# Optimization experiments

Hardware: AMD Instinct MI355X
Metric: run time of the kernel (lower is better)

The kernel has to match this reference:

```python
import jax, jax.numpy as jnp
import numpy as np

NUM_HEAD = 16
D_MODEL = 1024


def setup_inputs() -> dict:
    key = jax.random.key(0)
    ks = jax.random.split(key, 11)
    B, S, D = 2, 2048, D_MODEL
    scale = 1.0 / np.sqrt(D)
    inp = {
        "q": jax.random.normal(ks[0], (B, S, D), dtype=jnp.float32),
        "k": jax.random.normal(ks[1], (B, S, D), dtype=jnp.float32),
        "v": jax.random.normal(ks[2], (B, S, D), dtype=jnp.float32),
        "Wq": jax.random.normal(ks[3], (D, D), dtype=jnp.float32) * scale,
        "bq": jnp.zeros((D,), dtype=jnp.float32),
        "Wk": jax.random.normal(ks[4], (D, D), dtype=jnp.float32) * scale,
        "bk": jnp.zeros((D,), dtype=jnp.float32),
        "Wv": jax.random.normal(ks[5], (D, D), dtype=jnp.float32) * scale,
        "bv": jnp.zeros((D,), dtype=jnp.float32),
        "Wo": jax.random.normal(ks[6], (D, D), dtype=jnp.float32) * scale,
        "bo": jnp.zeros((D,), dtype=jnp.float32),
    }
    return inp


def _split_heads(x, num_head):
    B, S, D = x.shape
    return x.reshape(B, S, num_head, D // num_head).transpose(0, 2, 1, 3)  # [B,H,S,d]


def reference(q, k, v, Wq, bq, Wk, bk, Wv, bv, Wo, bo):
    H = NUM_HEAD
    qp = q @ Wq + bq
    kp = k @ Wk + bk  # computed but UNUSED, matching source bug
    vp = v @ Wv + bv
    # source bug: k := split_heads(v-projection)
    qh = _split_heads(qp, H)          # [B,H,S,d]
    kh = _split_heads(vp, H)          # [B,H,S,d]  (v-projection used as keys)
    vh = _split_heads(vp, H)          # [B,H,S,d]
    d = qh.shape[-1]
    scores = jnp.einsum('bhqd,bhkd->bhqk', qh, kh) / jnp.sqrt(jnp.asarray(d, qh.dtype))
    attn = jax.nn.softmax(scores, axis=-1)
    out = jnp.einsum('bhqk,bhkd->bhqd', attn, vh)  # [B,H,S,d]
    B, _, S, _ = out.shape
    out = out.transpose(0, 2, 1, 3).reshape(B, S, H * d)
    return out @ Wo + bo
```

## Files before the change

### kernel.cpp

```cpp
#include <hip/hip_runtime.h>
#include <hip/hip_bf16.h>

using bfrag  = __attribute__((ext_vector_type(8))) __bf16;
using f32x4  = __attribute__((ext_vector_type(4))) float;
using f32x16 = __attribute__((ext_vector_type(16))) float;
using v4u    = __attribute__((ext_vector_type(4))) unsigned int;
using v2u    = __attribute__((ext_vector_type(2))) unsigned int;

__device__ __forceinline__ ushort f2bf(float f) {
    union { float f; unsigned u; } c; c.f = f;
    return (ushort)((c.u + 0x7fffu + ((c.u >> 16) & 1u)) >> 16);
}

__device__ __forceinline__ float bf2f(ushort u) {
    union { unsigned u; float f; } c; c.u = (unsigned)u << 16; return c.f;
}

__device__ __forceinline__ unsigned pack_bf16x2(float lo, float hi) {
    union { __hip_bfloat162 h; unsigned u; } c;
    c.h = __float22bfloat162_rn(make_float2(lo, hi));
    return c.u;
}

__device__ __forceinline__ void gld_lds16(const ushort* g, ushort* l) {
    __builtin_amdgcn_global_load_lds(
        (const __attribute__((address_space(1))) void*)g,
        (__attribute__((address_space(3))) void*)l, 16, 0, 0);
}

__device__ __forceinline__ f32x16 mfma32(bfrag a, bfrag b, f32x16 c) {
    return __builtin_amdgcn_mfma_f32_32x32x16_bf16(a, b, c, 0, 0, 0);
}


__global__ void cvt_all(const float* __restrict__ s0, ushort* __restrict__ d0,
                        const float* __restrict__ s1, ushort* __restrict__ d1,
                        const float* __restrict__ s2, ushort* __restrict__ d2,
                        const float* __restrict__ q, ushort* __restrict__ qbf,
                        const float* __restrict__ v, ushort* __restrict__ vbf) {
    const int z = blockIdx.z;
    if (z < 3) {
        __shared__ float t[32][33];
        const float* src = z == 0 ? s0 : z == 1 ? s1 : s2;
        ushort* dst = z == 0 ? d0 : z == 1 ? d1 : d2;
        const int tx = threadIdx.x, ty = threadIdx.y;
        const int c0 = blockIdx.x * 32, r0 = blockIdx.y * 32;
        for (int i = ty; i < 32; i += 8) t[i][tx] = src[(size_t)(r0 + i) * 1024 + c0 + tx];
        __syncthreads();
        for (int i = ty; i < 32; i += 8) dst[(size_t)(c0 + i) * 1024 + r0 + tx] = f2bf(t[tx][i]);
    } else {
        const int tid = threadIdx.y * 32 + threadIdx.x;
        int i = ((z - 3) * 1024 + blockIdx.y * 32 + blockIdx.x) * 256 + tid;
        const float* s; ushort* d;
        if (i < 1048576) { s = q; d = qbf; } else { s = v; d = vbf; i -= 1048576; }
        float4 f = ((const float4*)s)[i];
        ((ushort4*)d)[i] = make_ushort4(f2bf(f.x), f2bf(f.y), f2bf(f.z), f2bf(f.w));
    }
}


__global__ __launch_bounds__(256, 3) void gemm_qv(
    const ushort* __restrict__ Aq, const ushort* __restrict__ Wq, const float* __restrict__ bq, ushort* __restrict__ Cq,
    const ushort* __restrict__ Av, const ushort* __restrict__ Wv, const float* __restrict__ bv, ushort* __restrict__ Cv,
    ushort* __restrict__ VPT, float qscale)
{
    __shared__ ushort SM[12288];
    const int z = blockIdx.z;
    const ushort* A  = z ? Av : Aq;
    const ushort* Bt = z ? Wv : Wq;
    const float* bias = z ? bv : bq;
    ushort* Cout = z ? Cv : Cq;
    const float scale = z ? 1.0f : qscale;

    const int tid = threadIdx.x;
    const int lane = tid & 63, w = tid >> 6;
    const int l15 = lane & 15, lg = lane >> 4;
    const int wr = w >> 1, wc = w & 1;
    const int bM = blockIdx.y, bN = blockIdx.x;

    const ushort* Ag = A + (size_t)bM * 64 * 1024;
    const ushort* Bg = Bt + (size_t)bN * 128 * 1024;
    const int ar = tid >> 2;
    const int cc = (tid & 3) * 8;

    auto STAGE = [&](int buf, int kt) {
        const int kk = kt * 32;
        gld_lds16(Ag + (size_t)ar * 1024 + kk + cc, &SM[buf * 2048 + tid * 8]);
#pragma unroll
        for (int i = 0; i < 2; ++i)
            gld_lds16(Bg + (size_t)(ar + i * 64) * 1024 + kk + cc,
                      &SM[4096 + buf * 4096 + (tid + i * 256) * 8]);
    };

    f32x4 acc[2][4];
#pragma unroll
    for (int m = 0; m < 2; ++m)
#pragma unroll
        for (int n = 0; n < 4; ++n) acc[m][n] = (f32x4){0.f, 0.f, 0.f, 0.f};

    STAGE(0, 0);
    __syncthreads();
    int cur = 0;
    for (int kt = 0; kt < 32; ++kt) {
        if (kt < 31) STAGE(cur ^ 1, kt + 1);
        bfrag aF[2], bF[4];
#pragma unroll
        for (int m = 0; m < 2; ++m)
            aF[m] = *(const bfrag*)&SM[cur * 2048 + (wr * 32 + m * 16 + l15) * 32 + lg * 8];
#pragma unroll
        for (int n = 0; n < 4; ++n)
            bF[n] = *(const bfrag*)&SM[4096 + cur * 4096 + (wc * 64 + n * 16 + l15) * 32 + lg * 8];
        __builtin_amdgcn_s_setprio(1);
#pragma unroll
        for (int m = 0; m < 2; ++m)
#pragma unroll
            for (int n = 0; n < 4; ++n)
                acc[m][n] = __builtin_amdgcn_mfma_f32_16x16x32_bf16(aF[m], bF[n], acc[m][n], 0, 0, 0);
        __builtin_amdgcn_s_setprio(0);
        if (kt < 31) {
            __syncthreads();
            cur ^= 1;
        }
    }

    __syncthreads();
#pragma unroll
    for (int m = 0; m < 2; ++m)
#pragma unroll
        for (int n = 0; n < 4; ++n) {
            const int lcol = wc * 64 + n * 16 + l15;
            const int gcol = bN * 128 + lcol;
            const float bv_ = bias[gcol];
#pragma unroll
            for (int j = 0; j < 4; ++j) {
                const int lrow = wr * 32 + m * 16 + lg * 4 + j;
                const float val = (acc[m][n][j] + bv_) * scale;
                const ushort hv = f2bf(val);
                Cout[(size_t)(bM * 64 + lrow) * 1024 + gcol] = hv;
                if (z) SM[lrow * 129 + lcol] = hv;
            }
        }

    if (z) {
        __syncthreads();
        const int b_ = (bM * 64) >> 11;
        const int s0 = (bM * 64) & 2047;
        const int h0 = bN * 2;
#pragma unroll
        for (int i = 0; i < 4; ++i) {
            const int c2 = i * 256 + tid;
            const int d128 = c2 >> 3;
            const int sb = (c2 & 7) * 8;
            union { ushort s[8]; v4u v; } tmp;
#pragma unroll
            for (int jj = 0; jj < 8; ++jj) {
                const int sl = sb + jj;
                const int js = (sl & ~15) | (sl & 3) | ((sl >> 1) & 4) | ((sl << 1) & 8);
                tmp.s[jj] = SM[js * 129 + d128];
            }
            ushort* dst = VPT + ((size_t)((b_ * 16 + h0 + (d128 >> 6)) * 64 + (d128 & 63))) * 2048 + s0 + sb;
            *(v4u*)dst = tmp.v;
        }
    }
}


__global__ __launch_bounds__(256, 3) void gemm_o(
    const ushort* __restrict__ Op0, const ushort* __restrict__ Op1,
    const float* __restrict__ Lp,
    const ushort* __restrict__ Bt, const float* __restrict__ bias,
    float* __restrict__ out)
{
    __shared__ ushort As[2][2048];
    __shared__ ushort Bs[2][4096];
    const int tid = threadIdx.x;
    const int lane = tid & 63, w = tid >> 6;
    const int l15 = lane & 15, lg = lane >> 4;
    const int wr = w >> 1, wc = w & 1;
    const int bM = blockIdx.y, bN = blockIdx.x;

    const ushort* Bg = Bt + (size_t)bN * 128 * 1024;
    const int ar = tid >> 2;
    const int cc = (tid & 3) * 8;
    const int grow = bM * 64 + ar;
    const int b_ = grow >> 11, s_ = grow & 2047;

    v4u aR, cR; float inv;
    auto LOAD_A = [&](int kt) {
        const int col = kt * 32 + cc;
        const int li = (b_ * 16 + (col >> 6)) * 2048 + s_;
        inv = 1.0f / (Lp[li] + Lp[65536 + li]);
        aR = *(const v4u*)(Op0 + (size_t)grow * 1024 + col);
        cR = *(const v4u*)(Op1 + (size_t)grow * 1024 + col);
    };
    auto WRITE_A = [&](int buf) {
        v4u o;
#pragma unroll
        for (int wd = 0; wd < 4; ++wd) {
            const float x0 = (bf2f((ushort)(aR[wd] & 0xffff)) + bf2f((ushort)(cR[wd] & 0xffff))) * inv;
            const float x1 = (bf2f((ushort)(aR[wd] >> 16))    + bf2f((ushort)(cR[wd] >> 16)))    * inv;
            o[wd] = pack_bf16x2(x0, x1);
        }
        *(v4u*)&As[buf][tid * 8] = o;
    };
    auto STAGE_B = [&](int buf, int kt) {
        const int kk = kt * 32;
#pragma unroll
        for (int i = 0; i < 2; ++i)
            gld_lds16(Bg + (size_t)(ar + i * 64) * 1024 + kk + cc, &Bs[buf][(tid + i * 256) * 8]);
    };

    f32x4 acc[2][4];
#pragma unroll
    for (int m = 0; m < 2; ++m)
#pragma unroll
        for (int n = 0; n < 4; ++n) acc[m][n] = (f32x4){0.f, 0.f, 0.f, 0.f};

    LOAD_A(0);
    STAGE_B(0, 0);
    WRITE_A(0);
    __syncthreads();
    int cur = 0;
    for (int kt = 0; kt < 32; ++kt) {
        if (kt < 31) {
            LOAD_A(kt + 1);
            STAGE_B(cur ^ 1, kt + 1);
        }
        bfrag aF[2], bF[4];
#pragma unroll
        for (int m = 0; m < 2; ++m) aF[m] = *(const bfrag*)&As[cur][(wr * 32 + m * 16 + l15) * 32 + lg * 8];
#pragma unroll
        for (int n = 0; n < 4; ++n) bF[n] = *(const bfrag*)&Bs[cur][(wc * 64 + n * 16 + l15) * 32 + lg * 8];
        __builtin_amdgcn_s_setprio(1);
#pragma unroll
        for (int m = 0; m < 2; ++m)
#pragma unroll
            for (int n = 0; n < 4; ++n)
                acc[m][n] = __builtin_amdgcn_mfma_f32_16x16x32_bf16(aF[m], bF[n], acc[m][n], 0, 0, 0);
        __builtin_amdgcn_s_setprio(0);
        if (kt < 31) {
            WRITE_A(cur ^ 1);
            __syncthreads();
            cur ^= 1;
        }
    }

#pragma unroll
    for (int m = 0; m < 2; ++m)
#pragma unroll
        for (int n = 0; n < 4; ++n) {
            const int gcol = bN * 128 + wc * 64 + n * 16 + l15;
            const float bv_ = bias[gcol];
#pragma unroll
            for (int j = 0; j < 4; ++j) {
                const int gr = bM * 64 + wr * 32 + m * 16 + lg * 4 + j;
                out[(size_t)gr * 1024 + gcol] = acc[m][n][j] + bv_;
            }
        }
}


__global__ __launch_bounds__(256, 2) void attn_kernel(
    const ushort* __restrict__ QP, const ushort* __restrict__ VP,
    const ushort* __restrict__ VPT, ushort* __restrict__ Opart, float* __restrict__ Lpart)
{
    __shared__ ushort Ks[2][4096];
    __shared__ ushort Vs[2][4096];
    const int tid = threadIdx.x;
    const int w = tid >> 6, lane = tid & 63;
    const int l31 = lane & 31, hi = lane >> 5;
    const int bh = blockIdx.x, qt = blockIdx.y, half = blockIdx.z;
    const int b = bh >> 4, h = bh & 15;
    const int qrow0 = qt * 256 + w * 64;
    const int k0 = half * 16;

    const int sr = lane >> 3;
    const int sc = ((lane & 7) ^ sr) * 8;
    const ushort* Kg = VP + (size_t)(b * 2048) * 1024 + h * 64 + sc;
    const ushort* Vg = VPT + (size_t)bh * 131072 + sc;

    auto STAGE = [&](int slot, int kt) {
#pragma unroll
        for (int i = 0; i < 2; ++i) {
            const int kb = w * 2 + i;
            const int r = kb * 8 + sr;
            gld_lds16(Kg + (size_t)(kt * 64 + r) * 1024, &Ks[slot][kb * 512]);
            gld_lds16(Vg + (size_t)r * 2048 + kt * 64, &Vs[slot][kb * 512]);
        }
    };

    const ushort* Qp = QP + ((size_t)(b * 2048 + qrow0 + l31)) * 1024 + h * 64 + hi * 8;
    bfrag qA[4], qBt[4];
#pragma unroll
    for (int ds = 0; ds < 4; ++ds) {
        qA[ds]  = *(const bfrag*)(Qp + ds * 16);
        qBt[ds] = *(const bfrag*)(Qp + 32 * 1024 + ds * 16);
    }

    f32x16 OA0, OA1, OB0, OB1;
#pragma unroll
    for (int r = 0; r < 16; ++r) { OA0[r] = 0.f; OA1[r] = 0.f; OB0[r] = 0.f; OB1[r] = 0.f; }
    float lrunA = 0.f, lrunB = 0.f;

    const int swz = (l31 & 7) << 4;
    const int cA = hi * 16;

    STAGE(0, k0);
    __syncthreads();

    auto SOFTMAX = [&](f32x16& S0, f32x16& S1, bfrag (&pB)[4], float& lrun) {
        float p[32];
#pragma unroll
        for (int r = 0; r < 16; ++r) {
            p[r]      = __builtin_amdgcn_exp2f(S0[r]);
            p[16 + r] = __builtin_amdgcn_exp2f(S1[r]);
        }
        float s8[8];
#pragma unroll
        for (int i = 0; i < 8; ++i) s8[i] = (p[i] + p[i + 8]) + (p[i + 16] + p[i + 24]);
        lrun += ((s8[0] + s8[1]) + (s8[2] + s8[3])) + ((s8[4] + s8[5]) + (s8[6] + s8[7]));
#pragma unroll
        for (int c = 0; c < 4; ++c) {
            union { v4u u; bfrag f; } cv;
#pragma unroll
            for (int wd = 0; wd < 4; ++wd)
                cv.u[wd] = pack_bf16x2(p[8 * c + 2 * wd], p[8 * c + 2 * wd + 1]);
            pB[c] = cv.f;
        }
    };

#pragma unroll 1
    for (int t = 0; t < 16; ++t) {
        if (t > 0) __syncthreads();
        if (t + 1 < 16) STAGE((t + 1) & 1, k0 + t + 1);
        const ushort* Kb_ = Ks[t & 1];
        const ushort* Vb_ = Vs[t & 1];

        bfrag k0f[4], k1f[4];
#pragma unroll
        for (int ds = 0; ds < 4; ++ds) {
            k0f[ds] = *(const bfrag*)&Kb_[(l31 * 128 + ((ds * 32 + cA) ^ swz)) >> 1];
            k1f[ds] = *(const bfrag*)&Kb_[((l31 + 32) * 128 + ((ds * 32 + cA) ^ swz)) >> 1];
        }
        f32x16 SA0, SA1, SB0, SB1;
#pragma unroll
        for (int r = 0; r < 16; ++r) { SA0[r] = -16.f; SA1[r] = -16.f; SB0[r] = -16.f; SB1[r] = -16.f; }
        __builtin_amdgcn_s_setprio(1);
#pragma unroll
        for (int ds = 0; ds < 4; ++ds) {
            SA0 = mfma32(k0f[ds], qA[ds], SA0);
            SA1 = mfma32(k1f[ds], qA[ds], SA1);
            SB0 = mfma32(k0f[ds], qBt[ds], SB0);
            SB1 = mfma32(k1f[ds], qBt[ds], SB1);
        }
        __builtin_amdgcn_s_setprio(0);

        bfrag pBA[4], pBB[4];
        SOFTMAX(SA0, SA1, pBA, lrunA);
        SOFTMAX(SB0, SB1, pBB, lrunB);

        bfrag vF0[4], vF1[4];
#pragma unroll
        for (int c = 0; c < 4; ++c) {
            vF0[c] = *(const bfrag*)&Vb_[(l31 * 128 + ((c * 32 + cA) ^ swz)) >> 1];
            vF1[c] = *(const bfrag*)&Vb_[((l31 + 32) * 128 + ((c * 32 + cA) ^ swz)) >> 1];
        }
        __builtin_amdgcn_s_setprio(1);
#pragma unroll
        for (int c = 0; c < 4; ++c) {
            OA0 = mfma32(vF0[c], pBA[c], OA0);
            OA1 = mfma32(vF1[c], pBA[c], OA1);
            OB0 = mfma32(vF0[c], pBB[c], OB0);
            OB1 = mfma32(vF1[c], pBB[c], OB1);
        }
        __builtin_amdgcn_s_setprio(0);
    }

    lrunA += __shfl_xor(lrunA, 32);
    lrunB += __shfl_xor(lrunB, 32);
    ushort* AoA = Opart + (size_t)half * 4194304
                + (size_t)(b * 2048 + qrow0 + l31) * 1024 + h * 64 + hi * 4;
    ushort* AoB = AoA + 32 * 1024;
#pragma unroll
    for (int t = 0; t < 2; ++t) {
#pragma unroll
        for (int g = 0; g < 4; ++g) {
            const float a0 = t ? OA1[4 * g + 0] : OA0[4 * g + 0];
            const float a1 = t ? OA1[4 * g + 1] : OA0[4 * g + 1];
            const float a2 = t ? OA1[4 * g + 2] : OA0[4 * g + 2];
            const float a3 = t ? OA1[4 * g + 3] : OA0[4 * g + 3];
            *(v2u*)(AoA + t * 32 + g * 8) = (v2u){pack_bf16x2(a0, a1), pack_bf16x2(a2, a3)};
            const float b0 = t ? OB1[4 * g + 0] : OB0[4 * g + 0];
            const float b1 = t ? OB1[4 * g + 1] : OB0[4 * g + 1];
            const float b2 = t ? OB1[4 * g + 2] : OB0[4 * g + 2];
            const float b3 = t ? OB1[4 * g + 3] : OB0[4 * g + 3];
            *(v2u*)(AoB + t * 32 + g * 8) = (v2u){pack_bf16x2(b0, b1), pack_bf16x2(b2, b3)};
        }
    }
    if (hi == 0) {
        Lpart[half * 65536 + bh * 2048 + qrow0 + l31] = lrunA;
        Lpart[half * 65536 + bh * 2048 + qrow0 + 32 + l31] = lrunB;
    }
}


extern "C" void kernel_launch(void* const* d_in, const int* in_sizes, int n_in,
                              void* d_out, int out_size, void* d_ws, size_t ws_size,
                              hipStream_t stream) {
    (void)in_sizes; (void)n_in; (void)out_size; (void)ws_size;
    const float* q  = (const float*)d_in[0];
    const float* v  = (const float*)d_in[2];
    const float* Wq = (const float*)d_in[3];
    const float* bq = (const float*)d_in[4];
    const float* Wv = (const float*)d_in[7];
    const float* bv = (const float*)d_in[8];
    const float* Wo = (const float*)d_in[9];
    const float* bo = (const float*)d_in[10];
    float* out = (float*)d_out;
    char* ws = (char*)d_ws;
    const size_t MB = 1ull << 20;
    ushort* qbf = (ushort*)(ws + 0);
    ushort* vbf = (ushort*)(ws + 8 * MB);
    ushort* WqT = (ushort*)(ws + 16 * MB);
    ushort* WvT = (ushort*)(ws + 18 * MB);
    ushort* WoT = (ushort*)(ws + 20 * MB);
    ushort* QPb = (ushort*)(ws + 22 * MB);
    ushort* VPb = (ushort*)(ws + 30 * MB);
    ushort* VPT = (ushort*)(ws + 38 * MB);

    ushort* Opart = (ushort*)(ws + 0);
    float*  Lpart = (float*)(ws + 16 * MB);

    cvt_all<<<dim3(32, 32, 11), dim3(32, 8), 0, stream>>>(
        Wq, WqT, Wv, WvT, Wo, WoT, q, qbf, v, vbf);

    const float qscale = 0.125f * 1.44269504088896340736f;
    gemm_qv<<<dim3(8, 64, 2), 256, 0, stream>>>(qbf, WqT, bq, QPb,
                                                vbf, WvT, bv, VPb, VPT, qscale);
    attn_kernel<<<dim3(32, 8, 2), 256, 0, stream>>>(QPb, VPb, VPT, Opart, Lpart);
    gemm_o<<<dim3(8, 64), 256, 0, stream>>>(Opart, Opart + 4194304, Lpart, WoT, bo, out);
}
```

Baseline: 124.1 us.

## Fuse fp32-to-bf16 activation conversion into the QV projection GEMM

The separate pass that converted q and v from fp32 to bf16 is removed. gemm_qv now loads fp32 A tiles into registers, packs them to bf16 and writes them to LDS, double-buffered alongside the async B loads. This drops one kernel's global read/write of the activations. In exchange, A data is read as fp32 by each N-block, and the load goes through registers instead of direct-to-LDS.

```diff
diff --git a/kernel.cpp b/kernel.cpp
--- a/kernel.cpp
+++ b/kernel.cpp
@@ -33,40 +33,29 @@
 }
 
 
-__global__ void cvt_all(const float* __restrict__ s0, ushort* __restrict__ d0,
-                        const float* __restrict__ s1, ushort* __restrict__ d1,
-                        const float* __restrict__ s2, ushort* __restrict__ d2,
-                        const float* __restrict__ q, ushort* __restrict__ qbf,
-                        const float* __restrict__ v, ushort* __restrict__ vbf) {
+__global__ void cvt_W(const float* __restrict__ s0, ushort* __restrict__ d0,
+                      const float* __restrict__ s1, ushort* __restrict__ d1,
+                      const float* __restrict__ s2, ushort* __restrict__ d2) {
+    __shared__ float t[32][33];
     const int z = blockIdx.z;
-    if (z < 3) {
-        __shared__ float t[32][33];
-        const float* src = z == 0 ? s0 : z == 1 ? s1 : s2;
-        ushort* dst = z == 0 ? d0 : z == 1 ? d1 : d2;
-        const int tx = threadIdx.x, ty = threadIdx.y;
-        const int c0 = blockIdx.x * 32, r0 = blockIdx.y * 32;
-        for (int i = ty; i < 32; i += 8) t[i][tx] = src[(size_t)(r0 + i) * 1024 + c0 + tx];
-        __syncthreads();
-        for (int i = ty; i < 32; i += 8) dst[(size_t)(c0 + i) * 1024 + r0 + tx] = f2bf(t[tx][i]);
-    } else {
-        const int tid = threadIdx.y * 32 + threadIdx.x;
-        int i = ((z - 3) * 1024 + blockIdx.y * 32 + blockIdx.x) * 256 + tid;
-        const float* s; ushort* d;
-        if (i < 1048576) { s = q; d = qbf; } else { s = v; d = vbf; i -= 1048576; }
-        float4 f = ((const float4*)s)[i];
-        ((ushort4*)d)[i] = make_ushort4(f2bf(f.x), f2bf(f.y), f2bf(f.z), f2bf(f.w));
-    }
+    const float* src = z == 0 ? s0 : z == 1 ? s1 : s2;
+    ushort* dst = z == 0 ? d0 : z == 1 ? d1 : d2;
+    const int tx = threadIdx.x, ty = threadIdx.y;
+    const int c0 = blockIdx.x * 32, r0 = blockIdx.y * 32;
+    for (int i = ty; i < 32; i += 8) t[i][tx] = src[(size_t)(r0 + i) * 1024 + c0 + tx];
+    __syncthreads();
+    for (int i = ty; i < 32; i += 8) dst[(size_t)(c0 + i) * 1024 + r0 + tx] = f2bf(t[tx][i]);
 }
 
 
 __global__ __launch_bounds__(256, 3) void gemm_qv(
-    const ushort* __restrict__ Aq, const ushort* __restrict__ Wq, const float* __restrict__ bq, ushort* __restrict__ Cq,
-    const ushort* __restrict__ Av, const ushort* __restrict__ Wv, const float* __restrict__ bv, ushort* __restrict__ Cv,
+    const float* __restrict__ Aqf, const ushort* __restrict__ Wq, const float* __restrict__ bq, ushort* __restrict__ Cq,
+    const float* __restrict__ Avf, const ushort* __restrict__ Wv, const float* __restrict__ bv, ushort* __restrict__ Cv,
     ushort* __restrict__ VPT, float qscale)
 {
     __shared__ ushort SM[12288];
     const int z = blockIdx.z;
-    const ushort* A  = z ? Av : Aq;
+    const float* Af = z ? Avf : Aqf;
     const ushort* Bt = z ? Wv : Wq;
     const float* bias = z ? bv : bq;
     ushort* Cout = z ? Cv : Cq;
@@ -78,14 +67,24 @@
     const int wr = w >> 1, wc = w & 1;
     const int bM = blockIdx.y, bN = blockIdx.x;
 
-    const ushort* Ag = A + (size_t)bM * 64 * 1024;
+    const float* Ag = Af + (size_t)bM * 64 * 1024;
     const ushort* Bg = Bt + (size_t)bN * 128 * 1024;
     const int ar = tid >> 2;
     const int cc = (tid & 3) * 8;
 
-    auto STAGE = [&](int buf, int kt) {
+    float4 a0R, a1R;
+    auto LOAD_A = [&](int kt) {
+        const float* src = Ag + (size_t)ar * 1024 + kt * 32 + cc;
+        a0R = *(const float4*)src;
+        a1R = *(const float4*)(src + 4);
+    };
+    auto WRITE_A = [&](int buf) {
+        v4u o = (v4u){pack_bf16x2(a0R.x, a0R.y), pack_bf16x2(a0R.z, a0R.w),
+                      pack_bf16x2(a1R.x, a1R.y), pack_bf16x2(a1R.z, a1R.w)};
+        *(v4u*)&SM[buf * 2048 + tid * 8] = o;
+    };
+    auto STAGE_B = [&](int buf, int kt) {
         const int kk = kt * 32;
-        gld_lds16(Ag + (size_t)ar * 1024 + kk + cc, &SM[buf * 2048 + tid * 8]);
 #pragma unroll
         for (int i = 0; i < 2; ++i)
             gld_lds16(Bg + (size_t)(ar + i * 64) * 1024 + kk + cc,
@@ -98,11 +97,16 @@
 #pragma unroll
         for (int n = 0; n < 4; ++n) acc[m][n] = (f32x4){0.f, 0.f, 0.f, 0.f};
 
-    STAGE(0, 0);
+    LOAD_A(0);
+    STAGE_B(0, 0);
+    WRITE_A(0);
     __syncthreads();
     int cur = 0;
     for (int kt = 0; kt < 32; ++kt) {
-        if (kt < 31) STAGE(cur ^ 1, kt + 1);
+        if (kt < 31) {
+            LOAD_A(kt + 1);
+            STAGE_B(cur ^ 1, kt + 1);
+        }
         bfrag aF[2], bF[4];
 #pragma unroll
         for (int m = 0; m < 2; ++m)
@@ -118,6 +122,7 @@
                 acc[m][n] = __builtin_amdgcn_mfma_f32_16x16x32_bf16(aF[m], bF[n], acc[m][n], 0, 0, 0);
         __builtin_amdgcn_s_setprio(0);
         if (kt < 31) {
+            WRITE_A(cur ^ 1);
             __syncthreads();
             cur ^= 1;
         }
@@ -419,24 +424,20 @@
     float* out = (float*)d_out;
     char* ws = (char*)d_ws;
     const size_t MB = 1ull << 20;
-    ushort* qbf = (ushort*)(ws + 0);
-    ushort* vbf = (ushort*)(ws + 8 * MB);
+    ushort* Opart = (ushort*)(ws + 0);
     ushort* WqT = (ushort*)(ws + 16 * MB);
     ushort* WvT = (ushort*)(ws + 18 * MB);
     ushort* WoT = (ushort*)(ws + 20 * MB);
     ushort* QPb = (ushort*)(ws + 22 * MB);
     ushort* VPb = (ushort*)(ws + 30 * MB);
     ushort* VPT = (ushort*)(ws + 38 * MB);
-
-    ushort* Opart = (ushort*)(ws + 0);
     float*  Lpart = (float*)(ws + 16 * MB);
 
-    cvt_all<<<dim3(32, 32, 11), dim3(32, 8), 0, stream>>>(
-        Wq, WqT, Wv, WvT, Wo, WoT, q, qbf, v, vbf);
+    cvt_W<<<dim3(32, 32, 3), dim3(32, 8), 0, stream>>>(Wq, WqT, Wv, WvT, Wo, WoT);
 
     const float qscale = 0.125f * 1.44269504088896340736f;
-    gemm_qv<<<dim3(8, 64, 2), 256, 0, stream>>>(qbf, WqT, bq, QPb,
-                                                vbf, WvT, bv, VPb, VPT, qscale);
+    gemm_qv<<<dim3(8, 64, 2), 256, 0, stream>>>(q, WqT, bq, QPb,
+                                                v, WvT, bv, VPb, VPT, qscale);
     attn_kernel<<<dim3(32, 8, 2), 256, 0, stream>>>(QPb, VPb, VPT, Opart, Lpart);
     gemm_o<<<dim3(8, 64), 256, 0, stream>>>(Opart, Opart + 4194304, Lpart, WoT, bo, out);
 }
```

Measured after the change: 128.7 us. +3.7%, slower.

## Split attention KV range four ways when workspace allows, generalize combine

Applied to the files above, without the earlier changes.

Templates the attention kernel on the number of key tiles per block and the output GEMM on the number of partial splits. When the workspace is large enough, it launches four KV splits of 8 tiles each instead of two of 16, doubling the grid to 2048 blocks, and relocates the buffers to make room. The gemm_o prologue sums all partial outputs and normalizers. This raises parallelism and occupancy in attention at the cost of more partial-output traffic in the combine GEMM.

```diff
diff --git a/kernel.cpp b/kernel.cpp
--- a/kernel.cpp
+++ b/kernel.cpp
@@ -165,9 +165,9 @@
 }
 
 
+template<int NSPLIT>
 __global__ __launch_bounds__(256, 3) void gemm_o(
-    const ushort* __restrict__ Op0, const ushort* __restrict__ Op1,
-    const float* __restrict__ Lp,
+    const ushort* __restrict__ Op, const float* __restrict__ Lp,
     const ushort* __restrict__ Bt, const float* __restrict__ bias,
     float* __restrict__ out)
 {
@@ -185,22 +185,30 @@
     const int grow = bM * 64 + ar;
     const int b_ = grow >> 11, s_ = grow & 2047;
 
-    v4u aR, cR; float inv;
+    float a8[8]; float linv;
     auto LOAD_A = [&](int kt) {
         const int col = kt * 32 + cc;
         const int li = (b_ * 16 + (col >> 6)) * 2048 + s_;
-        inv = 1.0f / (Lp[li] + Lp[65536 + li]);
-        aR = *(const v4u*)(Op0 + (size_t)grow * 1024 + col);
-        cR = *(const v4u*)(Op1 + (size_t)grow * 1024 + col);
+        float l = 0.f;
+#pragma unroll
+        for (int j = 0; j < 8; ++j) a8[j] = 0.f;
+#pragma unroll
+        for (int s = 0; s < NSPLIT; ++s) {
+            l += Lp[s * 65536 + li];
+            v4u r = *(const v4u*)(Op + (size_t)s * 4194304 + (size_t)grow * 1024 + col);
+#pragma unroll
+            for (int wd = 0; wd < 4; ++wd) {
+                a8[2 * wd]     += bf2f((ushort)(r[wd] & 0xffff));
+                a8[2 * wd + 1] += bf2f((ushort)(r[wd] >> 16));
+            }
+        }
+        linv = 1.0f / l;
     };
     auto WRITE_A = [&](int buf) {
         v4u o;
 #pragma unroll
-        for (int wd = 0; wd < 4; ++wd) {
-            const float x0 = (bf2f((ushort)(aR[wd] & 0xffff)) + bf2f((ushort)(cR[wd] & 0xffff))) * inv;
-            const float x1 = (bf2f((ushort)(aR[wd] >> 16))    + bf2f((ushort)(cR[wd] >> 16)))    * inv;
-            o[wd] = pack_bf16x2(x0, x1);
-        }
+        for (int wd = 0; wd < 4; ++wd)
+            o[wd] = pack_bf16x2(a8[2 * wd] * linv, a8[2 * wd + 1] * linv);
         *(v4u*)&As[buf][tid * 8] = o;
     };
     auto STAGE_B = [&](int buf, int kt) {
@@ -260,6 +268,7 @@
 }
 
 
+template<int NT>
 __global__ __launch_bounds__(256, 2) void attn_kernel(
     const ushort* __restrict__ QP, const ushort* __restrict__ VP,
     const ushort* __restrict__ VPT, ushort* __restrict__ Opart, float* __restrict__ Lpart)
@@ -272,7 +281,7 @@
     const int bh = blockIdx.x, qt = blockIdx.y, half = blockIdx.z;
     const int b = bh >> 4, h = bh & 15;
     const int qrow0 = qt * 256 + w * 64;
-    const int k0 = half * 16;
+    const int k0 = half * NT;
 
     const int sr = lane >> 3;
     const int sc = ((lane & 7) ^ sr) * 8;
@@ -330,9 +339,9 @@
     };
 
 #pragma unroll 1
-    for (int t = 0; t < 16; ++t) {
+    for (int t = 0; t < NT; ++t) {
         if (t > 0) __syncthreads();
-        if (t + 1 < 16) STAGE((t + 1) & 1, k0 + t + 1);
+        if (t + 1 < NT) STAGE((t + 1) & 1, k0 + t + 1);
         const ushort* Kb_ = Ks[t & 1];
         const ushort* Vb_ = Vs[t & 1];
 
@@ -407,7 +416,7 @@
 extern "C" void kernel_launch(void* const* d_in, const int* in_sizes, int n_in,
                               void* d_out, int out_size, void* d_ws, size_t ws_size,
                               hipStream_t stream) {
-    (void)in_sizes; (void)n_in; (void)out_size; (void)ws_size;
+    (void)in_sizes; (void)n_in; (void)out_size;
     const float* q  = (const float*)d_in[0];
     const float* v  = (const float*)d_in[2];
     const float* Wq = (const float*)d_in[3];
@@ -419,17 +428,29 @@
     float* out = (float*)d_out;
     char* ws = (char*)d_ws;
     const size_t MB = 1ull << 20;
+    const bool big = ws_size >= 59 * MB;
+
     ushort* qbf = (ushort*)(ws + 0);
     ushort* vbf = (ushort*)(ws + 8 * MB);
     ushort* WqT = (ushort*)(ws + 16 * MB);
     ushort* WvT = (ushort*)(ws + 18 * MB);
-    ushort* WoT = (ushort*)(ws + 20 * MB);
-    ushort* QPb = (ushort*)(ws + 22 * MB);
-    ushort* VPb = (ushort*)(ws + 30 * MB);
-    ushort* VPT = (ushort*)(ws + 38 * MB);
-
-    ushort* Opart = (ushort*)(ws + 0);
-    float*  Lpart = (float*)(ws + 16 * MB);
+
+    ushort *WoT, *QPb, *VPb, *VPT, *Opart; float* Lpart;
+    if (big) {
+        Opart = (ushort*)(ws + 0);
+        Lpart = (float*)(ws + 32 * MB);
+        WoT   = (ushort*)(ws + 33 * MB);
+        QPb   = (ushort*)(ws + 35 * MB);
+        VPb   = (ushort*)(ws + 43 * MB);
+        VPT   = (ushort*)(ws + 51 * MB);
+    } else {
+        Opart = (ushort*)(ws + 0);
+        Lpart = (float*)(ws + 16 * MB);
+        WoT   = (ushort*)(ws + 20 * MB);
+        QPb   = (ushort*)(ws + 22 * MB);
+        VPb   = (ushort*)(ws + 30 * MB);
+        VPT   = (ushort*)(ws + 38 * MB);
+    }
 
     cvt_all<<<dim3(32, 32, 11), dim3(32, 8), 0, stream>>>(
         Wq, WqT, Wv, WvT, Wo, WoT, q, qbf, v, vbf);
@@ -437,6 +458,11 @@
     const float qscale = 0.125f * 1.44269504088896340736f;
     gemm_qv<<<dim3(8, 64, 2), 256, 0, stream>>>(qbf, WqT, bq, QPb,
                                                 vbf, WvT, bv, VPb, VPT, qscale);
-    attn_kernel<<<dim3(32, 8, 2), 256, 0, stream>>>(QPb, VPb, VPT, Opart, Lpart);
-    gemm_o<<<dim3(8, 64), 256, 0, stream>>>(Opart, Opart + 4194304, Lpart, WoT, bo, out);
-}
+    if (big) {
+        attn_kernel<8><<<dim3(32, 8, 4), 256, 0, stream>>>(QPb, VPb, VPT, Opart, Lpart);
+        gemm_o<4><<<dim3(8, 64), 256, 0, stream>>>(Opart, Lpart, WoT, bo, out);
+    } else {
+        attn_kernel<16><<<dim3(32, 8, 2), 256, 0, stream>>>(QPb, VPb, VPT, Opart, Lpart);
+        gemm_o<2><<<dim3(8, 64), 256, 0, stream>>>(Opart, Lpart, WoT, bo, out);
+    }
+}
```

Measured after the change: 157.4 us. 1.27x slower.
